# Performance work log

Hardware: AMD Instinct MI355X
Metric: run time of the kernel (lower is better)

Reference implementation:

```python
import jax, jax.numpy as jnp
import numpy as np

B, S, H = 64, 2048, 512


def setup_inputs() -> dict:
    key = jax.random.key(0)
    ks = jax.random.split(key, 11)
    sc = 1.0 / np.sqrt(H)
    return {
        "encoder_output": jax.random.normal(ks[0], (B, S, H), jnp.float32),
        "decoder_hidden": jax.random.normal(ks[1], (B, H), jnp.float32),
        "coverage": jax.random.uniform(ks[2], (B, S), jnp.float32),
        # params (torch Linear: y = x @ W.T + b); we store W already transposed as [in, out]
        "Wh": jax.random.normal(ks[3], (H, H), jnp.float32) * sc,
        "bh": jax.random.normal(ks[4], (H,), jnp.float32) * sc,
        "Ws": jax.random.normal(ks[5], (H, H), jnp.float32) * sc,
        "bs": jax.random.normal(ks[6], (H,), jnp.float32) * sc,
        "Wc": jax.random.normal(ks[7], (1, H), jnp.float32) * sc,  # Linear(1, H)
        "bc": jax.random.normal(ks[8], (H,), jnp.float32) * sc,
        "v_w": jax.random.normal(ks[9], (H,), jnp.float32) * sc,   # Linear(H, 1) weight
        "v_b": jax.random.normal(ks[10], (1,), jnp.float32) * sc,
    }


def reference(encoder_output, decoder_hidden, coverage, Wh, bh, Ws, bs, Wc, bc, v_w, v_b):
    # encoder_feature: [B,S,H]
    enc_f = jnp.einsum('bsh,hk->bsk', encoder_output, Wh) + bh
    # decoder_feature: [B,1,H]
    dec_f = (decoder_hidden @ Ws + bs)[:, None, :]
    # coverage_feature: [B,S,H] = cov[...,None] @ Wc(1,H) + bc
    cov_f = coverage[:, :, None] * Wc[0] + bc
    feat = jnp.tanh(enc_f + dec_f + cov_f)          # [B,S,H]
    e_t = jnp.einsum('bsh,h->bs', feat, v_w) + v_b[0]  # [B,S]
    a_t = jax.nn.softmax(e_t, axis=-1)
    sum_coverage = coverage + a_t
    return a_t, sum_coverage
```

## Files before the change

### kernel.cpp

```cpp
#include <hip/hip_runtime.h>
#include <math.h>


#define B_ 64
#define S_ 2048
#define H_ 512
#define M_ (B_ * S_)

#define BN 128
#define PHASES 4
#define KH 256
#define RPB 256

typedef __attribute__((ext_vector_type(4))) float f32x4;
typedef __attribute__((ext_vector_type(8))) short s16x8;

__device__ __forceinline__ short f2bf(float f) {
    unsigned u = __float_as_uint(f);
    u += 0x7fffu + ((u >> 16) & 1u);
    return (short)(u >> 16);
}

__device__ __forceinline__ s16x8 cvt8(float4 a, float4 b) {
    s16x8 r;
    r[0] = f2bf(a.x); r[1] = f2bf(a.y); r[2] = f2bf(a.z); r[3] = f2bf(a.w);
    r[4] = f2bf(b.x); r[5] = f2bf(b.y); r[6] = f2bf(b.z); r[7] = f2bf(b.w);
    return r;
}

__device__ __forceinline__ float fast_tanh(float x) {
    return 1.0f - 2.0f / (__expf(2.0f * x) + 1.0f);
}

__global__ __launch_bounds__(256) void transpose_cast(
    const float* __restrict__ Wh, short* __restrict__ Bt) {
    __shared__ float tile[32][33];
    const int n0 = blockIdx.x * 32, k0 = blockIdx.y * 32;
    const int tx = threadIdx.x & 31, ty = threadIdx.x >> 5;
#pragma unroll
    for (int r = 0; r < 32; r += 8)
        tile[ty + r][tx] = Wh[(size_t)(k0 + ty + r) * H_ + n0 + tx];
    __syncthreads();
#pragma unroll
    for (int r = 0; r < 32; r += 8)
        Bt[(size_t)(n0 + ty + r) * H_ + k0 + tx] = f2bf(tile[tx][ty + r]);
}

__global__ __launch_bounds__(512) void dec_kernel(
    const float* __restrict__ dh, const float* __restrict__ Ws,
    const float* __restrict__ bs, const float* __restrict__ bh,
    const float* __restrict__ bc, float* __restrict__ D) {
    const int b = blockIdx.x;
    const int h = threadIdx.x;
    __shared__ float sdh[H_];
    sdh[h] = dh[b * H_ + h];
    __syncthreads();
    float acc = bs[h] + bh[h] + bc[h];
#pragma unroll 8
    for (int k = 0; k < H_; ++k)
        acc = fmaf(sdh[k], Ws[k * H_ + h], acc);
    D[b * H_ + h] = acc;
}

__global__ __launch_bounds__(512, 4) void gemm_fused(
    const float* __restrict__ A,
    const short* __restrict__ Bt,
    const float* __restrict__ cover,
    const float* __restrict__ Wc,
    const float* __restrict__ vw,
    const float* __restrict__ D,
    float* __restrict__ e_ws) {
    __shared__ __align__(16) short Bs[BN * KH];

    const int tid = threadIdx.x;
    const int w = tid >> 6;
    const int l = tid & 63;
    const int q = l >> 4;
    const int ml = l & 15;

    const int phase = blockIdx.x;
    const int n0 = phase * BN;
    const int row_blk = blockIdx.y * RPB;
    const int b = row_blk >> 11;
    const int r0 = row_blk + w * 32;

    f32x4 acc[2][8];
#pragma unroll
    for (int t = 0; t < 2; ++t)
#pragma unroll
        for (int u = 0; u < 8; ++u) acc[t][u] = (f32x4)0.0f;

    const float* ap0 = A + (size_t)(r0 + ml) * H_ + q * 8;
    const float* ap1 = ap0 + (size_t)16 * H_;
    float4 pa0 = *(const float4*)ap0;
    float4 pa1 = *(const float4*)(ap0 + 4);
    float4 pa2 = *(const float4*)ap1;
    float4 pa3 = *(const float4*)(ap1 + 4);
    ap0 += 32; ap1 += 32;

    const int sn = tid >> 2;
    const int scb = (tid & 3) * 8;
    const short* sg = Bt + (size_t)(n0 + sn) * H_ + scb * 8;
    short* sd = Bs + sn * KH;

    for (int half = 0; half < 2; ++half) {
        if (half) __syncthreads();
#pragma unroll
        for (int j = 0; j < 8; ++j) {
            const int c = scb + j;
            const int cs = c ^ (sn & 7);
            *(s16x8*)(sd + cs * 8) = *(const s16x8*)(sg + j * 8 + half * KH);
        }
        __syncthreads();

#pragma unroll
        for (int ks = 0; ks < 8; ++ks) {
            const s16x8 a0 = cvt8(pa0, pa1);
            const s16x8 a1 = cvt8(pa2, pa3);
            if (!(half == 1 && ks == 7)) {
                pa0 = *(const float4*)ap0;
                pa1 = *(const float4*)(ap0 + 4);
                pa2 = *(const float4*)ap1;
                pa3 = *(const float4*)(ap1 + 4);
                ap0 += 32; ap1 += 32;
            }
            const int cbase = ks * 4 + q;
#pragma unroll
            for (int uh = 0; uh < 2; ++uh) {
                s16x8 bfr[4];
#pragma unroll
                for (int v = 0; v < 4; ++v) {
                    const int n = (uh * 4 + v) * 16 + ml;
                    bfr[v] = *(const s16x8*)&Bs[n * KH + (cbase ^ (n & 7)) * 8];
                }
#pragma unroll
                for (int v = 0; v < 4; ++v) {
                    acc[0][uh * 4 + v] = __builtin_amdgcn_mfma_f32_16x16x32_bf16(
                        a0, bfr[v], acc[0][uh * 4 + v], 0, 0, 0);
                    acc[1][uh * 4 + v] = __builtin_amdgcn_mfma_f32_16x16x32_bf16(
                        a1, bfr[v], acc[1][uh * 4 + v], 0, 0, 0);
                }
            }
        }
    }

    float wc[8], vv[8], dd[8];
#pragma unroll
    for (int u = 0; u < 8; ++u) {
        const int n = n0 + u * 16 + ml;
        wc[u] = Wc[n];
        vv[u] = vw[n];
        dd[u] = D[b * H_ + n];
    }
#pragma unroll
    for (int t = 0; t < 2; ++t) {
        const int rb = r0 + t * 16 + q * 4;
        float p0 = 0.f, p1 = 0.f, p2 = 0.f, p3 = 0.f;
        const float cv0 = cover[rb + 0];
        const float cv1 = cover[rb + 1];
        const float cv2 = cover[rb + 2];
        const float cv3 = cover[rb + 3];
#pragma unroll
        for (int u = 0; u < 8; ++u) {
            p0 += vv[u] * fast_tanh(acc[t][u].x + fmaf(cv0, wc[u], dd[u]));
            p1 += vv[u] * fast_tanh(acc[t][u].y + fmaf(cv1, wc[u], dd[u]));
            p2 += vv[u] * fast_tanh(acc[t][u].z + fmaf(cv2, wc[u], dd[u]));
            p3 += vv[u] * fast_tanh(acc[t][u].w + fmaf(cv3, wc[u], dd[u]));
        }
#pragma unroll
        for (int s = 1; s < 16; s <<= 1) {
            p0 += __shfl_xor(p0, s, 64);
            p1 += __shfl_xor(p1, s, 64);
            p2 += __shfl_xor(p2, s, 64);
            p3 += __shfl_xor(p3, s, 64);
        }
        if (ml == 0) {
            float* dst = e_ws + (size_t)phase * M_ + rb;
            dst[0] = p0; dst[1] = p1; dst[2] = p2; dst[3] = p3;
        }
    }
}

__global__ __launch_bounds__(256) void softmax_kernel(
    const float* __restrict__ e_ws, const float* __restrict__ cover,
    const float* __restrict__ vb, float* __restrict__ out) {
    const int b = blockIdx.x;
    const int tid = threadIdx.x;
    const float vbv = vb[0];

    float e[8];
    float mx = -1e30f;
#pragma unroll
    for (int r = 0; r < 8; ++r) {
        const int idx = b * S_ + r * 256 + tid;
        e[r] = e_ws[idx] + e_ws[M_ + idx] + e_ws[2 * M_ + idx] +
               e_ws[3 * M_ + idx] + vbv;
        mx = fmaxf(mx, e[r]);
    }
#pragma unroll
    for (int off = 32; off >= 1; off >>= 1) mx = fmaxf(mx, __shfl_xor(mx, off, 64));

    __shared__ float sm[4], ss[4], sbc[2];
    const int wid = tid >> 6, lane = tid & 63;
    if (lane == 0) sm[wid] = mx;
    __syncthreads();
    if (tid == 0) sbc[0] = fmaxf(fmaxf(sm[0], sm[1]), fmaxf(sm[2], sm[3]));
    __syncthreads();
    mx = sbc[0];

    float ex[8];
    float sum = 0.0f;
#pragma unroll
    for (int r = 0; r < 8; ++r) {
        ex[r] = __expf(e[r] - mx);
        sum += ex[r];
    }
#pragma unroll
    for (int off = 32; off >= 1; off >>= 1) sum += __shfl_xor(sum, off, 64);
    if (lane == 0) ss[wid] = sum;
    __syncthreads();
    if (tid == 0) sbc[1] = ss[0] + ss[1] + ss[2] + ss[3];
    __syncthreads();
    const float inv = 1.0f / sbc[1];

#pragma unroll
    for (int r = 0; r < 8; ++r) {
        const int s = r * 256 + tid;
        const float a = ex[r] * inv;
        out[b * S_ + s] = a;
        out[M_ + b * S_ + s] = cover[b * S_ + s] + a;
    }
}

extern "C" void kernel_launch(void* const* d_in, const int* in_sizes, int n_in,
                              void* d_out, int out_size, void* d_ws, size_t ws_size,
                              hipStream_t stream) {
    const float* enc = (const float*)d_in[0];
    const float* dh  = (const float*)d_in[1];
    const float* cov = (const float*)d_in[2];
    const float* Wh  = (const float*)d_in[3];
    const float* bh  = (const float*)d_in[4];
    const float* Ws  = (const float*)d_in[5];
    const float* bs  = (const float*)d_in[6];
    const float* Wc  = (const float*)d_in[7];
    const float* bc  = (const float*)d_in[8];
    const float* vw  = (const float*)d_in[9];
    const float* vb  = (const float*)d_in[10];
    float* out = (float*)d_out;

    float* e_ws = (float*)d_ws;
    float* Dws  = e_ws + PHASES * M_;
    short* Whbt = (short*)(Dws + B_ * H_);

    transpose_cast<<<dim3(H_ / 32, H_ / 32), 256, 0, stream>>>(Wh, Whbt);
    dec_kernel<<<B_, 512, 0, stream>>>(dh, Ws, bs, bh, bc, Dws);
    dim3 g2(PHASES, M_ / RPB);
    gemm_fused<<<g2, 512, 0, stream>>>(enc, Whbt, cov, Wc, vw, Dws, e_ws);
    softmax_kernel<<<B_, 256, 0, stream>>>(e_ws, cov, vb, out);
}
```

Measured before the change: 542.4 us.

## Keep encoder rows in registers and loop over all output columns per block

Each block now loads its 128 encoder rows once, converts them to bf16 and holds them in registers. It then iterates over all eight 64-column chunks of Wh staged through LDS, accumulating the tanh·v reduction in place. This removes the fourfold re-read of the encoder tensor and the partial-sum workspace that softmax previously summed. It costs heavy register use, repeated Wh tile loads per block and lower occupancy.

```diff
diff --git a/kernel.cpp b/kernel.cpp
--- a/kernel.cpp
+++ b/kernel.cpp
@@ -7,10 +7,9 @@
 #define H_ 512
 #define M_ (B_ * S_)
 
-#define BN 128
-#define PHASES 4
-#define KH 256
-#define RPB 256
+#define RPB 128
+#define BN 64
+#define NPH 8
 
 typedef __attribute__((ext_vector_type(4))) float f32x4;
 typedef __attribute__((ext_vector_type(8))) short s16x8;
@@ -62,15 +61,15 @@
     D[b * H_ + h] = acc;
 }
 
-__global__ __launch_bounds__(512, 4) void gemm_fused(
+__global__ __launch_bounds__(256, 2) void gemm_fused(
     const float* __restrict__ A,
     const short* __restrict__ Bt,
     const float* __restrict__ cover,
     const float* __restrict__ Wc,
     const float* __restrict__ vw,
     const float* __restrict__ D,
-    float* __restrict__ e_ws) {
-    __shared__ __align__(16) short Bs[BN * KH];
+    float* __restrict__ e_t) {
+    __shared__ __align__(16) short Bs[BN * H_];
 
     const int tid = threadIdx.x;
     const int w = tid >> 6;
@@ -78,95 +77,101 @@
     const int q = l >> 4;
     const int ml = l & 15;
 
-    const int phase = blockIdx.x;
-    const int n0 = phase * BN;
-    const int row_blk = blockIdx.y * RPB;
+    const int row_blk = blockIdx.x * RPB;
     const int b = row_blk >> 11;
     const int r0 = row_blk + w * 32;
 
-    f32x4 acc[2][8];
+    s16x8 a[2][16];
+    {
+        const float* ap = A + (size_t)(r0 + ml) * H_ + q * 8;
+#pragma unroll
+        for (int kw = 0; kw < 16; ++kw) {
+#pragma unroll
+            for (int t = 0; t < 2; ++t) {
+                const float* p = ap + (size_t)t * 16 * H_ + kw * 32;
+                float4 x = *(const float4*)p;
+                float4 y = *(const float4*)(p + 4);
+                a[t][kw] = cvt8(x, y);
+            }
+        }
+    }
+
+    float cv[2][4];
 #pragma unroll
     for (int t = 0; t < 2; ++t)
 #pragma unroll
-        for (int u = 0; u < 8; ++u) acc[t][u] = (f32x4)0.0f;
-
-    const float* ap0 = A + (size_t)(r0 + ml) * H_ + q * 8;
-    const float* ap1 = ap0 + (size_t)16 * H_;
-    float4 pa0 = *(const float4*)ap0;
-    float4 pa1 = *(const float4*)(ap0 + 4);
-    float4 pa2 = *(const float4*)ap1;
-    float4 pa3 = *(const float4*)(ap1 + 4);
-    ap0 += 32; ap1 += 32;
+        for (int r = 0; r < 4; ++r)
+            cv[t][r] = cover[r0 + t * 16 + q * 4 + r];
 
     const int sn = tid >> 2;
-    const int scb = (tid & 3) * 8;
-    const short* sg = Bt + (size_t)(n0 + sn) * H_ + scb * 8;
-    short* sd = Bs + sn * KH;
-
-    for (int half = 0; half < 2; ++half) {
-        if (half) __syncthreads();
-#pragma unroll
-        for (int j = 0; j < 8; ++j) {
-            const int c = scb + j;
-            const int cs = c ^ (sn & 7);
-            *(s16x8*)(sd + cs * 8) = *(const s16x8*)(sg + j * 8 + half * KH);
+    const int sq = tid & 3;
+    const int sv = sn >> 4;
+    const int sml = sn & 15;
+    short* sdst0 = Bs + sv * 512 + (sq * 16 + (sml ^ (sq << 1))) * 8;
+    const int fb = (q * 16 + (ml ^ (q << 1))) * 8;
+
+    float ecur[2][4] = {};
+
+    for (int ph = 0; ph < NPH; ++ph) {
+        const short* sg = Bt + ((size_t)ph * BN + sn) * H_ + sq * 8;
+        if (ph) __syncthreads();
+#pragma unroll
+        for (int hv = 0; hv < 2; ++hv) {
+            s16x8 tmp[8];
+#pragma unroll
+            for (int j = 0; j < 8; ++j)
+                tmp[j] = *(const s16x8*)(sg + (hv * 8 + j) * 32);
+#pragma unroll
+            for (int j = 0; j < 8; ++j)
+                *(s16x8*)(sdst0 + (size_t)(hv * 8 + j) * 2048) = tmp[j];
         }
         __syncthreads();
 
-#pragma unroll
-        for (int ks = 0; ks < 8; ++ks) {
-            const s16x8 a0 = cvt8(pa0, pa1);
-            const s16x8 a1 = cvt8(pa2, pa3);
-            if (!(half == 1 && ks == 7)) {
-                pa0 = *(const float4*)ap0;
-                pa1 = *(const float4*)(ap0 + 4);
-                pa2 = *(const float4*)ap1;
-                pa3 = *(const float4*)(ap1 + 4);
-                ap0 += 32; ap1 += 32;
+        float wc[4], vv[4], dd[4];
+#pragma unroll
+        for (int v = 0; v < 4; ++v) {
+            const int n = ph * BN + v * 16 + ml;
+            wc[v] = Wc[n];
+            vv[v] = vw[n];
+            dd[v] = D[b * H_ + n];
+        }
+
+        f32x4 acc[2][4];
+#pragma unroll
+        for (int t = 0; t < 2; ++t)
+#pragma unroll
+            for (int v = 0; v < 4; ++v) acc[t][v] = (f32x4)0.0f;
+
+#pragma unroll
+        for (int kw = 0; kw < 16; ++kw) {
+            s16x8 bfr[4];
+#pragma unroll
+            for (int v = 0; v < 4; ++v)
+                bfr[v] = *(const s16x8*)&Bs[kw * 2048 + v * 512 + fb];
+#pragma unroll
+            for (int v = 0; v < 4; ++v) {
+                acc[0][v] = __builtin_amdgcn_mfma_f32_16x16x32_bf16(
+                    a[0][kw], bfr[v], acc[0][v], 0, 0, 0);
+                acc[1][v] = __builtin_amdgcn_mfma_f32_16x16x32_bf16(
+                    a[1][kw], bfr[v], acc[1][v], 0, 0, 0);
             }
-            const int cbase = ks * 4 + q;
-#pragma unroll
-            for (int uh = 0; uh < 2; ++uh) {
-                s16x8 bfr[4];
-#pragma unroll
-                for (int v = 0; v < 4; ++v) {
-                    const int n = (uh * 4 + v) * 16 + ml;
-                    bfr[v] = *(const s16x8*)&Bs[n * KH + (cbase ^ (n & 7)) * 8];
-                }
-#pragma unroll
-                for (int v = 0; v < 4; ++v) {
-                    acc[0][uh * 4 + v] = __builtin_amdgcn_mfma_f32_16x16x32_bf16(
-                        a0, bfr[v], acc[0][uh * 4 + v], 0, 0, 0);
-                    acc[1][uh * 4 + v] = __builtin_amdgcn_mfma_f32_16x16x32_bf16(
-                        a1, bfr[v], acc[1][uh * 4 + v], 0, 0, 0);
-                }
+        }
+
+#pragma unroll
+        for (int t = 0; t < 2; ++t) {
+#pragma unroll
+            for (int v = 0; v < 4; ++v) {
+                ecur[t][0] += vv[v] * fast_tanh(acc[t][v].x + fmaf(cv[t][0], wc[v], dd[v]));
+                ecur[t][1] += vv[v] * fast_tanh(acc[t][v].y + fmaf(cv[t][1], wc[v], dd[v]));
+                ecur[t][2] += vv[v] * fast_tanh(acc[t][v].z + fmaf(cv[t][2], wc[v], dd[v]));
+                ecur[t][3] += vv[v] * fast_tanh(acc[t][v].w + fmaf(cv[t][3], wc[v], dd[v]));
             }
         }
     }
 
-    float wc[8], vv[8], dd[8];
-#pragma unroll
-    for (int u = 0; u < 8; ++u) {
-        const int n = n0 + u * 16 + ml;
-        wc[u] = Wc[n];
-        vv[u] = vw[n];
-        dd[u] = D[b * H_ + n];
-    }
 #pragma unroll
     for (int t = 0; t < 2; ++t) {
-        const int rb = r0 + t * 16 + q * 4;
-        float p0 = 0.f, p1 = 0.f, p2 = 0.f, p3 = 0.f;
-        const float cv0 = cover[rb + 0];
-        const float cv1 = cover[rb + 1];
-        const float cv2 = cover[rb + 2];
-        const float cv3 = cover[rb + 3];
-#pragma unroll
-        for (int u = 0; u < 8; ++u) {
-            p0 += vv[u] * fast_tanh(acc[t][u].x + fmaf(cv0, wc[u], dd[u]));
-            p1 += vv[u] * fast_tanh(acc[t][u].y + fmaf(cv1, wc[u], dd[u]));
-            p2 += vv[u] * fast_tanh(acc[t][u].z + fmaf(cv2, wc[u], dd[u]));
-            p3 += vv[u] * fast_tanh(acc[t][u].w + fmaf(cv3, wc[u], dd[u]));
-        }
+        float p0 = ecur[t][0], p1 = ecur[t][1], p2 = ecur[t][2], p3 = ecur[t][3];
 #pragma unroll
         for (int s = 1; s < 16; s <<= 1) {
             p0 += __shfl_xor(p0, s, 64);
@@ -175,14 +180,14 @@
             p3 += __shfl_xor(p3, s, 64);
         }
         if (ml == 0) {
-            float* dst = e_ws + (size_t)phase * M_ + rb;
-            dst[0] = p0; dst[1] = p1; dst[2] = p2; dst[3] = p3;
+            float4 st = {p0, p1, p2, p3};
+            *(float4*)&e_t[r0 + t * 16 + q * 4] = st;
         }
     }
 }
 
 __global__ __launch_bounds__(256) void softmax_kernel(
-    const float* __restrict__ e_ws, const float* __restrict__ cover,
+    const float* __restrict__ e_t, const float* __restrict__ cover,
     const float* __restrict__ vb, float* __restrict__ out) {
     const int b = blockIdx.x;
     const int tid = threadIdx.x;
@@ -192,9 +197,7 @@
     float mx = -1e30f;
 #pragma unroll
     for (int r = 0; r < 8; ++r) {
-        const int idx = b * S_ + r * 256 + tid;
-        e[r] = e_ws[idx] + e_ws[M_ + idx] + e_ws[2 * M_ + idx] +
-               e_ws[3 * M_ + idx] + vbv;
+        e[r] = e_t[b * S_ + r * 256 + tid] + vbv;
         mx = fmaxf(mx, e[r]);
     }
 #pragma unroll
@@ -248,13 +251,12 @@
     const float* vb  = (const float*)d_in[10];
     float* out = (float*)d_out;
 
-    float* e_ws = (float*)d_ws;
-    float* Dws  = e_ws + PHASES * M_;
+    float* e_t  = (float*)d_ws;
+    float* Dws  = e_t + M_;
     short* Whbt = (short*)(Dws + B_ * H_);
 
     transpose_cast<<<dim3(H_ / 32, H_ / 32), 256, 0, stream>>>(Wh, Whbt);
     dec_kernel<<<B_, 512, 0, stream>>>(dh, Ws, bs, bh, bc, Dws);
-    dim3 g2(PHASES, M_ / RPB);
-    gemm_fused<<<g2, 512, 0, stream>>>(enc, Whbt, cov, Wc, vw, Dws, e_ws);
-    softmax_kernel<<<B_, 256, 0, stream>>>(e_ws, cov, vb, out);
-}
+    gemm_fused<<<M_ / RPB, 256, 0, stream>>>(enc, Whbt, cov, Wc, vw, Dws, e_t);
+    softmax_kernel<<<B_, 256, 0, stream>>>(e_t, cov, vb, out);
+}
```

Result: faster. 491.8 us (-9.3%).
